# Performance work log

Measured on AMD Instinct MI355X. Metric: run time of the kernel, lower is better.

Reference implementation:

```python
import jax, jax.numpy as jnp
import numpy as np

B, C, H, W = 4, 256, 64, 64
C8 = C // 8  # q/k projection dim = 32

def setup_inputs() -> dict:
    key = jax.random.key(0)
    ks = jax.random.split(key, 6)
    s = 0.02
    return {
        "x": jax.random.normal(ks[0], (B, C, H, W), dtype=jnp.float32),
        "wq": jax.random.normal(ks[1], (C8, C), dtype=jnp.float32) * s,
        "bq": jnp.zeros((C8,), dtype=jnp.float32),
        "wk": jax.random.normal(ks[2], (C8, C), dtype=jnp.float32) * s,
        "bk": jnp.zeros((C8,), dtype=jnp.float32),
        "wv": jax.random.normal(ks[3], (C, C), dtype=jnp.float32) * s,
        "bv": jnp.zeros((C,), dtype=jnp.float32),
        "wo": jax.random.normal(ks[4], (C, C), dtype=jnp.float32) * s,
        "bo": jnp.zeros((C,), dtype=jnp.float32),
        "scale": jnp.zeros((1,), dtype=jnp.float32),
    }

def reference(x, wq, bq, wk, bk, wv, bv, wo, bo, scale):
    b, c, h, w = x.shape
    n = h * w
    xf = x.reshape(b, c, n)  # (B, C, N)
    # 1x1 convs are channel-mixing GEMMs
    q = jnp.einsum('oc,bcn->bon', wq, xf) + bq[None, :, None]  # (B, C8, N)
    k = jnp.einsum('oc,bcn->bon', wk, xf) + bk[None, :, None]  # (B, C8, N)
    v = jnp.einsum('oc,bcn->bon', wv, xf) + bv[None, :, None]  # (B, C,  N)
    inv_sqrt = 1.0 / jnp.sqrt(jnp.asarray(c // 8, dtype=x.dtype))
    scores = jnp.einsum('bon,bom->bnm', q, k) * inv_sqrt  # (B, N, N): query n, key m
    attn = jax.nn.softmax(scores, axis=-1)
    # torch: bmm(value, attn^T) -> attended[:, :, n] = sum_m v[:, :, m] * attn[n, m]
    attended = jnp.einsum('bcm,bnm->bcn', v, attn)  # (B, C, N)
    out = jnp.einsum('oc,bcn->bon', wo, attended) + bo[None, :, None]
    out = out.reshape(b, c, h, w)
    return x + scale[0] * out
```

## Files before the change

kernel.cpp:

```cpp
#include <hip/hip_runtime.h>
#include <stdint.h>

#define B_ 4
#define C_ 256
#define C8_ 32
#define N_ 4096
#define LOG2E 1.4426950408889634f
#define INV_SQRT32 0.17677669529663689f
#define QSCALE (INV_SQRT32 * LOG2E)

typedef __bf16 bf16x8 __attribute__((ext_vector_type(8)));
typedef float f32x16 __attribute__((ext_vector_type(16)));
typedef unsigned int uint4v __attribute__((ext_vector_type(4)));

__device__ __forceinline__ uint16_t f2bf(float f) {
  uint32_t u = __builtin_bit_cast(uint32_t, f);
  return (uint16_t)((u + 0x7FFFu + ((u >> 16) & 1u)) >> 16);
}
__device__ __forceinline__ uint32_t pack2bf(float a, float b) {
  uint32_t ua = __builtin_bit_cast(uint32_t, a);
  uint32_t ub = __builtin_bit_cast(uint32_t, b);
  ua = (ua + 0x7FFFu + ((ua >> 16) & 1u)) >> 16;
  ub = (ub + 0x7FFFu + ((ub >> 16) & 1u)) & 0xFFFF0000u;
  return ua | ub;
}
__device__ __forceinline__ bf16x8 load_bf8(const uint16_t* p) {
  uint4v u = *(const uint4v*)p;
  return __builtin_bit_cast(bf16x8, u);
}
__device__ __forceinline__ f32x16 mfma32(bf16x8 a, bf16x8 b, f32x16 c) {
  return __builtin_amdgcn_mfma_f32_32x32x16_bf16(a, b, c, 0, 0, 0);
}
__device__ __forceinline__ f32x16 mfma32_f8(long a, long b, f32x16 c) {
  return __builtin_amdgcn_mfma_f32_32x32x16_fp8_fp8(a, b, c, 0, 0, 0);
}

__device__ __forceinline__ void pack_p_fp8(const float* P, int h, long& pa, long& pb) {
  uint32_t w0 = __builtin_amdgcn_cvt_pk_fp8_f32(P[0], P[1], 0, false);
  w0 = __builtin_amdgcn_cvt_pk_fp8_f32(P[2], P[3], w0, true);
  uint32_t w1 = __builtin_amdgcn_cvt_pk_fp8_f32(P[4], P[5], 0, false);
  w1 = __builtin_amdgcn_cvt_pk_fp8_f32(P[6], P[7], w1, true);
  uint32_t w2 = __builtin_amdgcn_cvt_pk_fp8_f32(P[8], P[9], 0, false);
  w2 = __builtin_amdgcn_cvt_pk_fp8_f32(P[10], P[11], w2, true);
  uint32_t w3 = __builtin_amdgcn_cvt_pk_fp8_f32(P[12], P[13], 0, false);
  w3 = __builtin_amdgcn_cvt_pk_fp8_f32(P[14], P[15], w3, true);
  uint32_t s0 = h ? w0 : w1;
  uint32_t s1 = h ? w2 : w3;
  uint32_t r0 = (uint32_t)__shfl_xor((int)s0, 32, 64);
  uint32_t r1 = (uint32_t)__shfl_xor((int)s1, 32, 64);
  uint32_t a0lo = h ? r0 : w0, a0hi = h ? w1 : r0;
  uint32_t a1lo = h ? r1 : w2, a1hi = h ? w3 : r1;
  pa = (long)(((uint64_t)a0hi << 32) | a0lo);
  pb = (long)(((uint64_t)a1hi << 32) | a1lo);
}

__global__ void k_wcast(const float* __restrict__ wq, const float* __restrict__ wk,
                        const float* __restrict__ wv, const float* __restrict__ wo,
                        uint16_t* __restrict__ wqb, uint16_t* __restrict__ wkb,
                        uint16_t* __restrict__ wvb, uint16_t* __restrict__ wob) {
  int i = blockIdx.x * 256 + threadIdx.x;
  if (i < 8192) {
    int o = i >> 8, c = i & 255;
    wqb[((size_t)(c >> 3) * 32 + o) * 8 + (c & 7)] = f2bf(wq[i]);
  } else if (i < 16384) {
    int j = i - 8192; int o = j >> 8, c = j & 255;
    wkb[((size_t)(c >> 3) * 32 + o) * 8 + (c & 7)] = f2bf(wk[j]);
  } else if (i < 81920) {
    int j = i - 16384; int o = j >> 8, c = j & 255;
    wvb[((size_t)(c >> 3) * 256 + o) * 8 + (c & 7)] = f2bf(wv[j]);
  } else {
    int j = i - 81920; int o = j >> 8, c = j & 255;
    wob[((size_t)(c >> 3) * 256 + o) * 8 + (c & 7)] = f2bf(wo[j]);
  }
}

__global__ __launch_bounds__(320) void k_proj_qkv(
    const float* __restrict__ x,
    const uint16_t* __restrict__ wqb, const float* __restrict__ bq,
    const uint16_t* __restrict__ wkb, const float* __restrict__ bk,
    const uint16_t* __restrict__ wvb, const float* __restrict__ bv,
    uint16_t* __restrict__ Qb, uint16_t* __restrict__ Kt, uint8_t* __restrict__ V8) {
  __shared__ uint4v xTv[32 * 32];
  int b = blockIdx.y;
  int n0 = blockIdx.x * 32;
  int tid = threadIdx.x;
  uint16_t* xT = (uint16_t*)xTv;

  if (tid < 256) {
    int r = tid >> 3;
    int l4 = (tid & 7) * 4;
#pragma unroll
    for (int p = 0; p < 8; p++) {
      int c = p * 32 + r;
      float4 v = *(const float4*)(x + ((size_t)b * C_ + c) * N_ + n0 + l4);
      int cg = c >> 3, cj = c & 7;
      xT[(cg * 32 + l4 + 0) * 8 + cj] = f2bf(v.x);
      xT[(cg * 32 + l4 + 1) * 8 + cj] = f2bf(v.y);
      xT[(cg * 32 + l4 + 2) * 8 + cj] = f2bf(v.z);
      xT[(cg * 32 + l4 + 3) * 8 + cj] = f2bf(v.w);
    }
  }
  __syncthreads();

  int wave = tid >> 6;
  int lane = tid & 63;
  int h = lane >> 5, ln = lane & 31;

  if (wave == 0) {
    f32x16 aq, ak;
#pragma unroll
    for (int i = 0; i < 16; i++) { aq[i] = 0.0f; ak[i] = 0.0f; }
#pragma unroll 4
    for (int c = 0; c < C_; c += 16) {
      bf16x8 bb = __builtin_bit_cast(bf16x8, xTv[(c / 8 + h) * 32 + ln]);
      aq = mfma32(load_bf8(wqb + ((size_t)(c / 8 + h) * 32 + ln) * 8), bb, aq);
      ak = mfma32(load_bf8(wkb + ((size_t)(c / 8 + h) * 32 + ln) * 8), bb, ak);
    }
#pragma unroll
    for (int g = 0; g < 4; g++) {
      int row = g * 8 + h * 4;
      uint2 pq, pk;
      pq.x = pack2bf((aq[4 * g + 0] + bq[row + 0]) * QSCALE,
                     (aq[4 * g + 1] + bq[row + 1]) * QSCALE);
      pq.y = pack2bf((aq[4 * g + 2] + bq[row + 2]) * QSCALE,
                     (aq[4 * g + 3] + bq[row + 3]) * QSCALE);
      *(uint2*)(Qb + ((size_t)b * N_ + n0 + ln) * C8_ + row) = pq;
      pk.x = pack2bf(ak[4 * g + 0] + bk[row + 0], ak[4 * g + 1] + bk[row + 1]);
      pk.y = pack2bf(ak[4 * g + 2] + bk[row + 2], ak[4 * g + 3] + bk[row + 3]);
      *(uint2*)(Kt + ((size_t)(b * 4 + g) * N_ + n0 + ln) * 8 + h * 4) = pk;
    }
  } else {
    int o0 = (wave - 1) * 64;
    f32x16 a0, a1;
#pragma unroll
    for (int i = 0; i < 16; i++) { a0[i] = 0.0f; a1[i] = 0.0f; }
#pragma unroll 4
    for (int c = 0; c < C_; c += 16) {
      bf16x8 bb = __builtin_bit_cast(bf16x8, xTv[(c / 8 + h) * 32 + ln]);
      a0 = mfma32(load_bf8(wvb + ((size_t)(c / 8 + h) * 256 + o0 + ln) * 8), bb, a0);
      a1 = mfma32(load_bf8(wvb + ((size_t)(c / 8 + h) * 256 + o0 + 32 + ln) * 8), bb, a1);
    }
    int kg = b * 512 + (n0 >> 3) + (ln >> 3);
    int j = ln & 7;
#pragma unroll
    for (int r = 0; r < 16; r++) {
      int row = (r & 3) + 8 * (r >> 2) + 4 * h;
      float v0 = a0[r] + bv[o0 + row];
      float v1 = a1[r] + bv[o0 + 32 + row];
      int p0 = __builtin_amdgcn_cvt_pk_fp8_f32(v0, v0, 0, false);
      int p1 = __builtin_amdgcn_cvt_pk_fp8_f32(v1, v1, 0, false);
      V8[((size_t)kg * 256 + o0 + row) * 8 + j] = (uint8_t)(p0 & 0xff);
      V8[((size_t)kg * 256 + o0 + 32 + row) * 8 + j] = (uint8_t)(p1 & 0xff);
    }
  }
}

__global__ __launch_bounds__(512, 4) void k_attn(
    const uint16_t* __restrict__ Qb, const uint16_t* __restrict__ Kt,
    const uint8_t* __restrict__ V8, const uint16_t* __restrict__ Wob,
    const float* __restrict__ bo, const float* __restrict__ x,
    const float* __restrict__ scale, float* __restrict__ out) {
  __shared__ uint32_t sO[8][2][8][64];
  __shared__ uint4v aTv[32 * 32];
  __shared__ float sl[4][32];

  int bx = blockIdx.x;
  int b = bx >> 1;
  int qt = blockIdx.y + 64 * (bx & 1);
  int wave = threadIdx.x >> 6;
  int kw = wave >> 1, cw = wave & 1;
  int lane = threadIdx.x & 63;
  int h = lane >> 5, ln = lane & 31;
  int qi = qt * 32 + ln;

  const uint16_t* qrow = Qb + ((size_t)b * N_ + qi) * C8_;
  bf16x8 qf1 = load_bf8(qrow + h * 8);
  bf16x8 qf2 = load_bf8(qrow + 16 + h * 8);
  const uint16_t* k1base = Kt + ((size_t)(b * 4 + h) * N_) * 8;
  const uint16_t* k2base = Kt + ((size_t)(b * 4 + 2 + h) * N_) * 8;

  f32x16 O[4];
#pragma unroll
  for (int t = 0; t < 4; t++)
#pragma unroll
    for (int r = 0; r < 16; r++) O[t][r] = 0.0f;
  float lsum = 0.0f;
  const uint8_t* vbase = V8 + (size_t)(b * 512) * 2048 + cw * 1024 + ln * 8;

  int m_lo = kw * 1024;
  bf16x8 ka1 = load_bf8(k1base + (size_t)(m_lo + ln) * 8);
  bf16x8 ka2 = load_bf8(k2base + (size_t)(m_lo + ln) * 8);

  for (int m0 = m_lo; m0 < m_lo + 1024; m0 += 32) {
    int mp = (m0 + 32) & (N_ - 1);
    bf16x8 kn1 = load_bf8(k1base + (size_t)(mp + ln) * 8);
    bf16x8 kn2 = load_bf8(k2base + (size_t)(mp + ln) * 8);

    f32x16 S;
#pragma unroll
    for (int i = 0; i < 16; i++) S[i] = 0.0f;
    S = mfma32(ka1, qf1, S);
    S = mfma32(ka2, qf2, S);

    float P[16];
#pragma unroll
    for (int r = 0; r < 16; r++) {
      P[r] = __builtin_amdgcn_exp2f(fminf(S[r], 7.5f));
    }
    if (cw == 0) {
#pragma unroll
      for (int r = 0; r < 16; r++) lsum += P[r];
    }
    long pa, pb;
    pack_p_fp8(P, h, pa, pb);

    const uint8_t* vp = vbase + (size_t)((m0 >> 3) + h) * 2048;
#pragma unroll
    for (int t = 0; t < 4; t++) {
      uint2 u1 = *(const uint2*)(vp + t * 256);
      uint2 u2 = *(const uint2*)(vp + 4096 + t * 256);
      long va = (long)(((uint64_t)u1.y << 32) | u1.x);
      long vc = (long)(((uint64_t)u2.y << 32) | u2.x);
      O[t] = mfma32_f8(va, pa, O[t]);
      O[t] = mfma32_f8(vc, pb, O[t]);
    }
    ka1 = kn1; ka2 = kn2;
  }
  if (cw == 0) {
    lsum += __shfl_xor(lsum, 32, 64);
    if (h == 0) sl[kw][ln] = lsum;
  }

#pragma unroll
  for (int rr = 0; rr < 2; rr++) {
    if (rr) __syncthreads();
#pragma unroll
    for (int t2 = 0; t2 < 2; t2++) {
      int t = rr * 2 + t2;
#pragma unroll
      for (int i = 0; i < 8; i++)
        sO[wave][t2][i][lane] = pack2bf(O[t][2 * i], O[t][2 * i + 1]);
    }
    __syncthreads();
    if (wave < 4) {
      int cw2 = wave >> 1, t2 = wave & 1;
      int gt = cw2 * 4 + rr * 2 + t2;
      float acc[16];
#pragma unroll
      for (int r = 0; r < 16; r++) acc[r] = 0.0f;
#pragma unroll
      for (int k = 0; k < 4; k++) {
        int src = k * 2 + cw2;
#pragma unroll
        for (int i = 0; i < 8; i++) {
          uint32_t u = sO[src][t2][i][lane];
          acc[2 * i]     += __builtin_bit_cast(float, u << 16);
          acc[2 * i + 1] += __builtin_bit_cast(float, u & 0xFFFF0000u);
        }
      }
      float lg = sl[0][ln] + sl[1][ln] + sl[2][ln] + sl[3][ln];
      float inv = 1.0f / lg;
      uint2* aT2 = (uint2*)aTv;
#pragma unroll
      for (int g = 0; g < 4; g++) {
        uint2 pr;
        pr.x = pack2bf(acc[4 * g + 0] * inv, acc[4 * g + 1] * inv);
        pr.y = pack2bf(acc[4 * g + 2] * inv, acc[4 * g + 3] * inv);
        aT2[((gt * 4 + g) * 32 + ln) * 2 + h] = pr;
      }
    }
  }
  __syncthreads();

  int o0 = wave * 32;
  f32x16 acc;
#pragma unroll
  for (int i = 0; i < 16; i++) acc[i] = 0.0f;
#pragma unroll 4
  for (int c = 0; c < C_; c += 16) {
    bf16x8 a = load_bf8(Wob + ((size_t)(c / 8 + h) * 256 + o0 + ln) * 8);
    bf16x8 bb = __builtin_bit_cast(bf16x8, aTv[(c / 8 + h) * 32 + ln]);
    acc = mfma32(a, bb, acc);
  }
  float s = scale[0];
#pragma unroll
  for (int r = 0; r < 16; r++) {
    int row = (r & 3) + 8 * (r >> 2) + 4 * h;
    int o = o0 + row;
    size_t idx = ((size_t)b * C_ + o) * N_ + qi;
    out[idx] = x[idx] + s * (acc[r] + bo[o]);
  }
}

extern "C" void kernel_launch(void* const* d_in, const int* in_sizes, int n_in,
                              void* d_out, int out_size, void* d_ws, size_t ws_size,
                              hipStream_t stream) {
  const float* x  = (const float*)d_in[0];
  const float* wq = (const float*)d_in[1];
  const float* bq = (const float*)d_in[2];
  const float* wk = (const float*)d_in[3];
  const float* bk = (const float*)d_in[4];
  const float* wv = (const float*)d_in[5];
  const float* bv = (const float*)d_in[6];
  const float* wo = (const float*)d_in[7];
  const float* bo = (const float*)d_in[8];
  const float* scale = (const float*)d_in[9];
  float* out = (float*)d_out;

  char* w = (char*)d_ws;
  uint16_t* Qb  = (uint16_t*)(w);
  uint16_t* Kt  = (uint16_t*)(w + (1u << 20));
  uint8_t*  V8  = (uint8_t*)(w + (2u << 20));
  uint16_t* Wqb = (uint16_t*)(w + (6u << 20));
  uint16_t* Wkb = Wqb + 32 * 256;
  uint16_t* Wvb = Wkb + 32 * 256;
  uint16_t* Wob = Wvb + 256 * 256;

  k_wcast<<<576, 256, 0, stream>>>(wq, wk, wv, wo, Wqb, Wkb, Wvb, Wob);
  k_proj_qkv<<<dim3(N_ / 32, B_), 320, 0, stream>>>(x, Wqb, bq, Wkb, bk, Wvb, bv,
                                                    Qb, Kt, V8);
  k_attn<<<dim3(8, 64), 512, 0, stream>>>(Qb, Kt, V8, Wob, bo, x, scale, out);
}
```

Baseline: 152.5 us.

## Split attention work by output channels per wave, sharing P tiles via LDS

```diff
diff --git a/kernel.cpp b/kernel.cpp
--- a/kernel.cpp
+++ b/kernel.cpp
@@ -33,25 +33,6 @@
 }
 __device__ __forceinline__ f32x16 mfma32_f8(long a, long b, f32x16 c) {
   return __builtin_amdgcn_mfma_f32_32x32x16_fp8_fp8(a, b, c, 0, 0, 0);
-}
-
-__device__ __forceinline__ void pack_p_fp8(const float* P, int h, long& pa, long& pb) {
-  uint32_t w0 = __builtin_amdgcn_cvt_pk_fp8_f32(P[0], P[1], 0, false);
-  w0 = __builtin_amdgcn_cvt_pk_fp8_f32(P[2], P[3], w0, true);
-  uint32_t w1 = __builtin_amdgcn_cvt_pk_fp8_f32(P[4], P[5], 0, false);
-  w1 = __builtin_amdgcn_cvt_pk_fp8_f32(P[6], P[7], w1, true);
-  uint32_t w2 = __builtin_amdgcn_cvt_pk_fp8_f32(P[8], P[9], 0, false);
-  w2 = __builtin_amdgcn_cvt_pk_fp8_f32(P[10], P[11], w2, true);
-  uint32_t w3 = __builtin_amdgcn_cvt_pk_fp8_f32(P[12], P[13], 0, false);
-  w3 = __builtin_amdgcn_cvt_pk_fp8_f32(P[14], P[15], w3, true);
-  uint32_t s0 = h ? w0 : w1;
-  uint32_t s1 = h ? w2 : w3;
-  uint32_t r0 = (uint32_t)__shfl_xor((int)s0, 32, 64);
-  uint32_t r1 = (uint32_t)__shfl_xor((int)s1, 32, 64);
-  uint32_t a0lo = h ? r0 : w0, a0hi = h ? w1 : r0;
-  uint32_t a1lo = h ? r1 : w2, a1hi = h ? w3 : r1;
-  pa = (long)(((uint64_t)a0hi << 32) | a0lo);
-  pb = (long)(((uint64_t)a1hi << 32) | a1lo);
 }
 
 __global__ void k_wcast(const float* __restrict__ wq, const float* __restrict__ wk,
@@ -160,15 +141,14 @@
     const uint8_t* __restrict__ V8, const uint16_t* __restrict__ Wob,
     const float* __restrict__ bo, const float* __restrict__ x,
     const float* __restrict__ scale, float* __restrict__ out) {
-  __shared__ uint32_t sO[8][2][8][64];
+  __shared__ uint32_t Pl[2][2048];
   __shared__ uint4v aTv[32 * 32];
-  __shared__ float sl[4][32];
+  __shared__ float sl[8][32];
 
   int bx = blockIdx.x;
   int b = bx >> 1;
   int qt = blockIdx.y + 64 * (bx & 1);
   int wave = threadIdx.x >> 6;
-  int kw = wave >> 1, cw = wave & 1;
   int lane = threadIdx.x & 63;
   int h = lane >> 5, ln = lane & 31;
   int qi = qt * 32 + ln;
@@ -179,22 +159,23 @@
   const uint16_t* k1base = Kt + ((size_t)(b * 4 + h) * N_) * 8;
   const uint16_t* k2base = Kt + ((size_t)(b * 4 + 2 + h) * N_) * 8;
 
-  f32x16 O[4];
-#pragma unroll
-  for (int t = 0; t < 4; t++)
-#pragma unroll
-    for (int r = 0; r < 16; r++) O[t][r] = 0.0f;
+  int o0 = wave * 32;
+  const uint8_t* vbase =
+      V8 + (size_t)(b * 512) * 2048 + (size_t)h * 2048 + (size_t)(o0 + ln) * 8;
+
+  f32x16 O;
+#pragma unroll
+  for (int r = 0; r < 16; r++) O[r] = 0.0f;
   float lsum = 0.0f;
-  const uint8_t* vbase = V8 + (size_t)(b * 512) * 2048 + cw * 1024 + ln * 8;
-
-  int m_lo = kw * 1024;
-  bf16x8 ka1 = load_bf8(k1base + (size_t)(m_lo + ln) * 8);
-  bf16x8 ka2 = load_bf8(k2base + (size_t)(m_lo + ln) * 8);
-
-  for (int m0 = m_lo; m0 < m_lo + 1024; m0 += 32) {
-    int mp = (m0 + 32) & (N_ - 1);
-    bf16x8 kn1 = load_bf8(k1base + (size_t)(mp + ln) * 8);
-    bf16x8 kn2 = load_bf8(k2base + (size_t)(mp + ln) * 8);
+
+  const int K0 = wave * 32;
+  bf16x8 ka1 = load_bf8(k1base + (size_t)(K0 + ln) * 8);
+  bf16x8 ka2 = load_bf8(k2base + (size_t)(K0 + ln) * 8);
+
+  for (int c = 0; c < 16; ++c) {
+    int kbn = ((c + 1) & 15) * 256 + K0;
+    bf16x8 kn1 = load_bf8(k1base + (size_t)(kbn + ln) * 8);
+    bf16x8 kn2 = load_bf8(k2base + (size_t)(kbn + ln) * 8);
 
     f32x16 S;
 #pragma unroll
@@ -204,82 +185,64 @@
 
     float P[16];
 #pragma unroll
-    for (int r = 0; r < 16; r++) {
-      P[r] = __builtin_amdgcn_exp2f(fminf(S[r], 7.5f));
-    }
-    if (cw == 0) {
-#pragma unroll
-      for (int r = 0; r < 16; r++) lsum += P[r];
-    }
-    long pa, pb;
-    pack_p_fp8(P, h, pa, pb);
-
-    const uint8_t* vp = vbase + (size_t)((m0 >> 3) + h) * 2048;
-#pragma unroll
-    for (int t = 0; t < 4; t++) {
-      uint2 u1 = *(const uint2*)(vp + t * 256);
-      uint2 u2 = *(const uint2*)(vp + 4096 + t * 256);
+    for (int r = 0; r < 16; r++) P[r] = __builtin_amdgcn_exp2f(fminf(S[r], 7.5f));
+    float l0 = 0.0f, l1 = 0.0f;
+#pragma unroll
+    for (int r = 0; r < 8; r++) { l0 += P[r]; l1 += P[r + 8]; }
+    lsum += l0 + l1;
+
+    uint32_t w0 = __builtin_amdgcn_cvt_pk_fp8_f32(P[0], P[1], 0, false);
+    w0 = __builtin_amdgcn_cvt_pk_fp8_f32(P[2], P[3], w0, true);
+    uint32_t w1 = __builtin_amdgcn_cvt_pk_fp8_f32(P[4], P[5], 0, false);
+    w1 = __builtin_amdgcn_cvt_pk_fp8_f32(P[6], P[7], w1, true);
+    uint32_t w2 = __builtin_amdgcn_cvt_pk_fp8_f32(P[8], P[9], 0, false);
+    w2 = __builtin_amdgcn_cvt_pk_fp8_f32(P[10], P[11], w2, true);
+    uint32_t w3 = __builtin_amdgcn_cvt_pk_fp8_f32(P[12], P[13], 0, false);
+    w3 = __builtin_amdgcn_cvt_pk_fp8_f32(P[14], P[15], w3, true);
+    uint32_t* pw = &Pl[c & 1][wave * 256 + ln * 2 + h];
+    pw[0] = w0; pw[64] = w1; pw[128] = w2; pw[192] = w3;
+
+    __syncthreads();
+
+    const uint8_t* vp = vbase + (size_t)c * 65536;
+    const uint32_t* pb = &Pl[c & 1][h * 64 + ln * 2];
+    __builtin_amdgcn_s_setprio(1);
+#pragma unroll 4
+    for (int g = 0; g < 16; ++g) {
+      uint2 u1 = *(const uint2*)(vp + (size_t)g * 4096);
+      uint2 pu = *(const uint2*)(pb + g * 128);
       long va = (long)(((uint64_t)u1.y << 32) | u1.x);
-      long vc = (long)(((uint64_t)u2.y << 32) | u2.x);
-      O[t] = mfma32_f8(va, pa, O[t]);
-      O[t] = mfma32_f8(vc, pb, O[t]);
-    }
+      long pa = (long)(((uint64_t)pu.y << 32) | pu.x);
+      O = mfma32_f8(va, pa, O);
+    }
+    __builtin_amdgcn_s_setprio(0);
     ka1 = kn1; ka2 = kn2;
   }
-  if (cw == 0) {
-    lsum += __shfl_xor(lsum, 32, 64);
-    if (h == 0) sl[kw][ln] = lsum;
-  }
-
-#pragma unroll
-  for (int rr = 0; rr < 2; rr++) {
-    if (rr) __syncthreads();
-#pragma unroll
-    for (int t2 = 0; t2 < 2; t2++) {
-      int t = rr * 2 + t2;
-#pragma unroll
-      for (int i = 0; i < 8; i++)
-        sO[wave][t2][i][lane] = pack2bf(O[t][2 * i], O[t][2 * i + 1]);
-    }
-    __syncthreads();
-    if (wave < 4) {
-      int cw2 = wave >> 1, t2 = wave & 1;
-      int gt = cw2 * 4 + rr * 2 + t2;
-      float acc[16];
-#pragma unroll
-      for (int r = 0; r < 16; r++) acc[r] = 0.0f;
-#pragma unroll
-      for (int k = 0; k < 4; k++) {
-        int src = k * 2 + cw2;
-#pragma unroll
-        for (int i = 0; i < 8; i++) {
-          uint32_t u = sO[src][t2][i][lane];
-          acc[2 * i]     += __builtin_bit_cast(float, u << 16);
-          acc[2 * i + 1] += __builtin_bit_cast(float, u & 0xFFFF0000u);
-        }
-      }
-      float lg = sl[0][ln] + sl[1][ln] + sl[2][ln] + sl[3][ln];
-      float inv = 1.0f / lg;
-      uint2* aT2 = (uint2*)aTv;
-#pragma unroll
-      for (int g = 0; g < 4; g++) {
-        uint2 pr;
-        pr.x = pack2bf(acc[4 * g + 0] * inv, acc[4 * g + 1] * inv);
-        pr.y = pack2bf(acc[4 * g + 2] * inv, acc[4 * g + 3] * inv);
-        aT2[((gt * 4 + g) * 32 + ln) * 2 + h] = pr;
-      }
-    }
-  }
+
+  lsum += __shfl_xor(lsum, 32, 64);
+  if (h == 0) sl[wave][ln] = lsum;
   __syncthreads();
-
-  int o0 = wave * 32;
+  float lg = 0.0f;
+#pragma unroll
+  for (int w = 0; w < 8; w++) lg += sl[w][ln];
+  float inv = 1.0f / lg;
+  uint2* aT2 = (uint2*)aTv;
+#pragma unroll
+  for (int g = 0; g < 4; ++g) {
+    uint2 pr2;
+    pr2.x = pack2bf(O[4 * g + 0] * inv, O[4 * g + 1] * inv);
+    pr2.y = pack2bf(O[4 * g + 2] * inv, O[4 * g + 3] * inv);
+    aT2[((wave * 4 + g) * 32 + ln) * 2 + h] = pr2;
+  }
+  __syncthreads();
+
   f32x16 acc;
 #pragma unroll
   for (int i = 0; i < 16; i++) acc[i] = 0.0f;
 #pragma unroll 4
-  for (int c = 0; c < C_; c += 16) {
-    bf16x8 a = load_bf8(Wob + ((size_t)(c / 8 + h) * 256 + o0 + ln) * 8);
-    bf16x8 bb = __builtin_bit_cast(bf16x8, aTv[(c / 8 + h) * 32 + ln]);
+  for (int cc = 0; cc < C_; cc += 16) {
+    bf16x8 a = load_bf8(Wob + ((size_t)(cc / 8 + h) * 256 + o0 + ln) * 8);
+    bf16x8 bb = __builtin_bit_cast(bf16x8, aTv[(cc / 8 + h) * 32 + ln]);
     acc = mfma32(a, bb, acc);
   }
   float s = scale[0];
```

After: 148.8 us. 1.02x faster.
